# Kernel tuning notes

Measured on AMD Instinct MI355X. Metric: run time of the kernel, lower is better.

The kernel has to match this reference:

```python
import jax, jax.numpy as jnp
import numpy as np


def bilinear_resize(x, out_h, out_w):
    # x: [B, C, H, W]; matches torch F.interpolate(mode='bilinear', align_corners=False)
    B, C, H, W = x.shape
    ry = jnp.clip((jnp.arange(out_h, dtype=jnp.float32) + 0.5) * (H / out_h) - 0.5, 0.0, H - 1)
    rx = jnp.clip((jnp.arange(out_w, dtype=jnp.float32) + 0.5) * (W / out_w) - 0.5, 0.0, W - 1)
    y0 = jnp.floor(ry).astype(jnp.int32); y1 = jnp.minimum(y0 + 1, H - 1)
    x0 = jnp.floor(rx).astype(jnp.int32); x1 = jnp.minimum(x0 + 1, W - 1)
    wy = (ry - y0)[:, None]  # [out_h,1]
    wx = (rx - x0)[None, :]  # [1,out_w]
    r0 = x[:, :, y0, :]; r1 = x[:, :, y1, :]
    v00 = r0[:, :, :, x0]; v01 = r0[:, :, :, x1]
    v10 = r1[:, :, :, x0]; v11 = r1[:, :, :, x1]
    return (v00 * (1 - wx) + v01 * wx) * (1 - wy) + (v10 * (1 - wx) + v11 * wx) * wy


def setup_inputs() -> dict:
    key0 = jax.random.key(0)
    ks = jax.random.split(key0, 16)
    B, N, C, H = 2, 300, 256, 8
    hw_lvl = np.array([[64, 64], [32, 32], [16, 16]], dtype=np.int64)
    L = int((hw_lvl[:, 0] * hw_lvl[:, 1]).sum())  # 5376
    p = lambda k, sh: (0.02 * jax.random.normal(k, sh, dtype=jnp.float32))
    return {
        'query': jax.random.normal(ks[0], (B, N, C), dtype=jnp.float32),
        'key': jax.random.normal(ks[1], (B, L, C), dtype=jnp.float32),
        'value': jax.random.normal(ks[2], (B, L, C), dtype=jnp.float32),
        'key_padding_mask': jnp.zeros((B, L), dtype=bool),
        'hw_lvl': hw_lvl,
        'Wq': p(ks[3], (C, C)), 'Wk': p(ks[4], (C, C)), 'Wv': p(ks[5], (C, C)),
        'Wp': p(ks[6], (C, C)), 'bp': jnp.zeros((C,), jnp.float32),
        'W1': p(ks[7], (H, H)), 'b1': jnp.zeros((H,), jnp.float32),
        'W2': p(ks[8], (H, H)), 'b2': jnp.zeros((H,), jnp.float32),
        'W3': p(ks[9], (H, H)), 'b3': jnp.zeros((H,), jnp.float32),
        'Wm': p(ks[10], (3 * H, 1)), 'bm': jnp.zeros((1,), jnp.float32),
    }


def reference(query, key, value, key_padding_mask, hw_lvl,
              Wq, Wk, Wv, Wp, bp, W1, b1, W2, b2, W3, b3, Wm, bm):
    hw = np.asarray(hw_lvl)
    h1, wd1 = int(hw[0, 0]), int(hw[0, 1])
    h2, wd2 = int(hw[1, 0]), int(hw[1, 1])
    h3, wd3 = int(hw[2, 0]), int(hw[2, 1])
    w1 = h1 * wd1
    w2 = w1 + h2 * wd2
    B, N, C = query.shape
    L = key.shape[1]
    H = W1.shape[0]
    scale = (C // H) ** -0.5

    q = (query @ Wq).reshape(B, N, H, C // H)
    k = (key @ Wk).reshape(B, L, H, C // H)
    v = (value @ Wv).reshape(B, L, H, C // H)
    attn = jnp.einsum('bnhd,blhd->bhnl', q, k) * scale  # [B,H,N,L]

    ap = attn.transpose(0, 2, 3, 1)  # [B,N,L,H]
    f1 = jax.nn.relu(ap[:, :, :w1] @ W1 + b1)                      # [B,N,w1,H]
    f2 = jax.nn.relu(ap[:, :, w1:w2] @ W2 + b2)                    # [B,N,h2*wd2,H]
    f3 = jax.nn.relu(ap[:, :, w2:] @ W3 + b3)                      # [B,N,h3*wd3,H]
    f2 = f2.transpose(0, 1, 3, 2).reshape(B * N, H, h2, wd2)
    f3 = f3.transpose(0, 1, 3, 2).reshape(B * N, H, h3, wd3)
    f2 = bilinear_resize(f2, h1, wd1).transpose(0, 2, 3, 1).reshape(B, N, w1, H)
    f3 = bilinear_resize(f3, h1, wd1).transpose(0, 2, 3, 1).reshape(B, N, w1, H)
    new_feats = jnp.concatenate([f1, f2, f3], axis=-1)             # [B,N,w1,3H]
    mask = jax.nn.relu(new_feats @ Wm + bm)                        # [B,N,w1,1]

    aw = jax.nn.softmax(attn, axis=-1)                             # [B,H,N,L]
    x = jnp.einsum('bhnl,blhd->bnhd', aw, v).reshape(B, N, C)
    x = x @ Wp + bp
    return x, mask
```

## Files before the change

### kernel.cpp

```cpp
#include <hip/hip_runtime.h>
#include <hip/hip_bf16.h>

typedef __hip_bfloat16 bf16;
typedef __attribute__((ext_vector_type(8))) short short8v;
typedef __attribute__((ext_vector_type(8))) unsigned short ushort8v;
typedef __attribute__((ext_vector_type(4))) unsigned short ushort4v;
typedef __attribute__((ext_vector_type(4))) float float4v;

__device__ __forceinline__ float bfu2f(unsigned short u) {
    union { unsigned int i; float f; } v; v.i = ((unsigned int)u) << 16; return v.f;
}
__device__ __forceinline__ unsigned short f2bfu_rn(float x) {
    union { float f; unsigned int i; } u; u.f = x;
    unsigned int r = (u.i + 0x7FFFu + ((u.i >> 16) & 1u)) >> 16;
    return (unsigned short)r;
}

__global__ __launch_bounds__(256) void cast_wt(
    const float* __restrict__ Wq, const float* __restrict__ Wk,
    const float* __restrict__ Wv, const float* __restrict__ Wp,
    unsigned short* __restrict__ wt)
{
    __shared__ unsigned short tile[64][72];
    const float* W = (blockIdx.z == 0) ? Wq : (blockIdx.z == 1) ? Wk
                   : (blockIdx.z == 2) ? Wv : Wp;
    unsigned short* WT = wt + (size_t)blockIdx.z * 65536;
    const int t = threadIdx.x;
    const int k0 = blockIdx.x * 64, n0 = blockIdx.y * 64;
    {
        const int r = t >> 2, cseg = (t & 3) * 16;
        const float* src = W + (size_t)(k0 + r) * 256 + n0 + cseg;
        #pragma unroll
        for (int j = 0; j < 16; ++j) tile[r][cseg + j] = f2bfu_rn(src[j]);
    }
    __syncthreads();
    {
        const int ch = t & 63, lq = t >> 6;
        ushort8v o0, o1;
        #pragma unroll
        for (int i = 0; i < 8; ++i) o0[i] = tile[lq * 16 + i][ch];
        #pragma unroll
        for (int i = 0; i < 8; ++i) o1[i] = tile[lq * 16 + 8 + i][ch];
        unsigned short* dst = WT + (size_t)(n0 + ch) * 256 + k0 + lq * 16;
        *(ushort8v*)(dst)     = o0;
        *(ushort8v*)(dst + 8) = o1;
    }
}

__device__ __forceinline__ void proj_core(
    const float* __restrict__ aptr, const unsigned short* __restrict__ Wt,
    int nc0, int m16, int quad, float4v acc[8])
{
    #pragma unroll
    for (int i = 0; i < 8; ++i) acc[i] = (float4v){0.f, 0.f, 0.f, 0.f};
    #pragma unroll
    for (int ks = 0; ks < 8; ++ks) {
        float4 a0 = *(const float4*)(aptr + ks * 32);
        float4 a1 = *(const float4*)(aptr + ks * 32 + 4);
        short8v af;
        af[0] = (short)f2bfu_rn(a0.x); af[1] = (short)f2bfu_rn(a0.y);
        af[2] = (short)f2bfu_rn(a0.z); af[3] = (short)f2bfu_rn(a0.w);
        af[4] = (short)f2bfu_rn(a1.x); af[5] = (short)f2bfu_rn(a1.y);
        af[6] = (short)f2bfu_rn(a1.z); af[7] = (short)f2bfu_rn(a1.w);
        #pragma unroll
        for (int i = 0; i < 8; ++i) {
            short8v bfr = *(const short8v*)(Wt + (size_t)(nc0 + i * 16 + m16) * 256 + ks * 32 + quad * 8);
            acc[i] = __builtin_amdgcn_mfma_f32_16x16x32_bf16(af, bfr, acc[i], 0, 0, 0);
        }
    }
}

__global__ __launch_bounds__(256) void proj_all(
    const float* __restrict__ q, const float* __restrict__ k, const float* __restrict__ v,
    const unsigned short* __restrict__ wt,
    unsigned short* __restrict__ qb, unsigned short* __restrict__ kb,
    unsigned short* __restrict__ vt)
{
    const int t = threadIdx.x;
    const int wave = t >> 6, lane = t & 63;
    const int m16 = lane & 15, quad = lane >> 4;
    const int msub = (wave & 1) * 16;
    const int nc0 = (wave >> 1) * 128;
    const int bx = blockIdx.x;

    float4v acc[8];
    if (bx < 19) {
        const int m0 = bx * 32;
        const int arow = min(m0 + msub + m16, 599);
        proj_core(q + (size_t)arow * 256 + quad * 8, wt, nc0, m16, quad, acc);
        #pragma unroll
        for (int i = 0; i < 8; ++i)
            #pragma unroll
            for (int r = 0; r < 4; ++r) {
                int m = m0 + msub + quad * 4 + r;
                if (m < 600)
                    qb[(size_t)m * 256 + nc0 + i * 16 + m16] = f2bfu_rn(acc[i][r]);
            }
    } else if (bx < 355) {
        const int m0 = (bx - 19) * 32;
        proj_core(k + (size_t)(m0 + msub + m16) * 256 + quad * 8, wt + 65536, nc0, m16, quad, acc);
        #pragma unroll
        for (int i = 0; i < 8; ++i)
            #pragma unroll
            for (int r = 0; r < 4; ++r) {
                int m = m0 + msub + quad * 4 + r;
                kb[(size_t)m * 256 + nc0 + i * 16 + m16] = f2bfu_rn(acc[i][r]);
            }
    } else {
        const int m0 = (bx - 355) * 32;
        proj_core(v + (size_t)(m0 + msub + m16) * 256 + quad * 8, wt + 131072, nc0, m16, quad, acc);
        const int bb = (m0 >= 5376) ? 1 : 0;
        const int lcol = m0 - bb * 5376 + msub + quad * 4;
        #pragma unroll
        for (int i = 0; i < 8; ++i) {
            const int ch = nc0 + i * 16 + m16;
            ushort4v p;
            #pragma unroll
            for (int r = 0; r < 4; ++r) p[r] = f2bfu_rn(acc[i][r]);
            *(ushort4v*)(vt + (size_t)(bb * 256 + ch) * 5376 + lcol) = p;
        }
    }
}

__global__ __launch_bounds__(512) void attn_fused(
    const unsigned short* __restrict__ qb, const unsigned short* __restrict__ kb,
    const unsigned short* __restrict__ vt,
    unsigned short* __restrict__ attn, float* __restrict__ xbp, float* __restrict__ Sp)
{
    __shared__ unsigned short probs[8][16 * 104];
    __shared__ float partial[8][64][9];
    __shared__ float SrowP[8][16];

    const int t = threadIdx.x;
    const int wave = t >> 6, lane = t & 63;

    const int i0 = blockIdx.x;
    const int c = i0 & 7;
    int m = i0 >> 3;
    const int half = (m >= 133) ? 1 : 0;
    const int bh = c * 2 + half;
    m -= half * 133;
    const int n0 = (m % 19) * 16;
    const int zz = m / 19;

    const int b = bh >> 3, h = bh & 7;
    const int m16 = lane & 15, quad = lane >> 4;
    const float scale = 0.17677669529663687f;

    const unsigned short* qp = qb + (size_t)(b * 300 + min(n0 + m16, 299)) * 256 + h * 32 + quad * 8;
    const short8v qfrag = *(const short8v*)qp;

    const unsigned short* kbase = kb + (size_t)(b * 5376) * 256 + h * 32 + quad * 8;
    const unsigned short* vt0 = vt + (size_t)(b * 256 + h * 32 + m16) * 5376;
    const unsigned short* vt1 = vt0 + (size_t)16 * 5376;

    unsigned short* pw = &probs[wave][0];
    const int lc = zz * 768 + wave * 96;

    float4v c0 = {0.f, 0.f, 0.f, 0.f};
    float4v c1 = {0.f, 0.f, 0.f, 0.f};
    float sm = 0.f;

    #pragma unroll
    for (int i = 0; i < 6; ++i) {
        const int lcol = lc + i * 16 + m16;
        short8v kf = *(const short8v*)(kbase + (size_t)lcol * 256);
        float4v c = {0.f, 0.f, 0.f, 0.f};
        c = __builtin_amdgcn_mfma_f32_16x16x32_bf16(kf, qfrag, c, 0, 0, 0);
        ushort4v pk;
        #pragma unroll
        for (int r = 0; r < 4; ++r) pk[r] = f2bfu_rn(c[r] * scale);
        *(ushort4v*)(pw + m16 * 104 + i * 16 + quad * 4) = pk;
    }

    {
        const int row = lane >> 2;
        const int n = n0 + row;
        if (n < 300) {
            unsigned short* gdst = attn + ((size_t)(b * 300 + n) * 8 + h) * 5376 + lc;
            const unsigned short* lsrc = pw + row * 104;
            #pragma unroll
            for (int it = 0; it < 3; ++it) {
                const int colk = (lane & 3) * 8 + it * 32;
                *(ushort8v*)(gdst + colk) = *(const ushort8v*)(lsrc + colk);
            }
        }
    }

    #pragma unroll
    for (int step = 0; step < 3; ++step) {
        const int lloc = step * 32 + quad * 8;
        ushort8v ua = *(const ushort8v*)(pw + m16 * 104 + lloc);
        short8v af;
        #pragma unroll
        for (int j = 0; j < 8; ++j) {
            float e = __expf(bfu2f(ua[j]));
            sm += e;
            af[j] = (short)f2bfu_rn(e);
        }
        const int lg = lc + lloc;
        short8v b0 = *(const short8v*)(vt0 + lg);
        short8v b1 = *(const short8v*)(vt1 + lg);
        c0 = __builtin_amdgcn_mfma_f32_16x16x32_bf16(af, b0, c0, 0, 0, 0);
        c1 = __builtin_amdgcn_mfma_f32_16x16x32_bf16(af, b1, c1, 0, 0, 0);
    }

    sm += __shfl_xor(sm, 16);
    sm += __shfl_xor(sm, 32);
    if (lane < 16) SrowP[wave][lane] = sm;
    #pragma unroll
    for (int j = 0; j < 4; ++j) {
        partial[wave][lane][j]     = c0[j];
        partial[wave][lane][4 + j] = c1[j];
    }
    __syncthreads();

    if (t < 64) {
        float acc[8] = {0.f, 0.f, 0.f, 0.f, 0.f, 0.f, 0.f, 0.f};
        #pragma unroll
        for (int w = 0; w < 8; ++w)
            #pragma unroll
            for (int j = 0; j < 8; ++j) acc[j] += partial[w][t][j];

        const int d = t & 15, q = t >> 4;
        float* xplane = xbp + (size_t)zz * 153600;
        float* splane = Sp + (size_t)zz * 4800;
        #pragma unroll
        for (int r = 0; r < 4; ++r) {
            const int row = q * 4 + r;
            const int nn = n0 + row;
            if (nn < 300) {
                float S = 0.f;
                #pragma unroll
                for (int w = 0; w < 8; ++w) S += SrowP[w][row];
                if (d == 0) splane[(size_t)(b * 300 + nn) * 8 + h] = S;
                float* o = xplane + (size_t)(b * 300 + nn) * 256 + h * 32 + d;
                o[0]  = acc[r];
                o[16] = acc[4 + r];
            }
        }
    }
}

__global__ __launch_bounds__(256) void proj_out(
    const float* __restrict__ xbp, const float* __restrict__ Sp,
    const unsigned short* __restrict__ Wtp,
    const float* __restrict__ bp, float* __restrict__ out)
{
    const int t = threadIdx.x;
    const int wave = t >> 6, lane = t & 63;
    const int m16 = lane & 15, quad = lane >> 4;
    const int msub = (wave & 1) * 16;
    const int nc0 = (wave >> 1) * 128;
    const int m0 = blockIdx.x * 32;

    const int arow = min(m0 + msub + m16, 599);
    const float* a0p = xbp + (size_t)arow * 256 + quad * 8;

    float4v acc[8];
    #pragma unroll
    for (int i = 0; i < 8; ++i) acc[i] = (float4v){0.f, 0.f, 0.f, 0.f};

    #pragma unroll
    for (int ks = 0; ks < 8; ++ks) {
        float S = 0.f;
        #pragma unroll
        for (int z = 0; z < 7; ++z) S += Sp[(size_t)z * 4800 + (size_t)arow * 8 + ks];
        const float rS = 1.0f / S;
        float a[8];
        #pragma unroll
        for (int half = 0; half < 2; ++half) {
            const float* p = a0p + ks * 32 + half * 4;
            float sx = 0.f, sy = 0.f, sz = 0.f, sw = 0.f;
            #pragma unroll
            for (int z = 0; z < 7; ++z) {
                float4 x = *(const float4*)(p + (size_t)z * 153600);
                sx += x.x; sy += x.y; sz += x.z; sw += x.w;
            }
            a[half * 4 + 0] = sx * rS;
            a[half * 4 + 1] = sy * rS;
            a[half * 4 + 2] = sz * rS;
            a[half * 4 + 3] = sw * rS;
        }
        short8v af;
        #pragma unroll
        for (int j = 0; j < 8; ++j) af[j] = (short)f2bfu_rn(a[j]);
        #pragma unroll
        for (int i = 0; i < 8; ++i) {
            short8v bfr = *(const short8v*)(Wtp + (size_t)(nc0 + i * 16 + m16) * 256 + ks * 32 + quad * 8);
            acc[i] = __builtin_amdgcn_mfma_f32_16x16x32_bf16(af, bfr, acc[i], 0, 0, 0);
        }
    }

    #pragma unroll
    for (int i = 0; i < 8; ++i) {
        const float bv = bp[nc0 + i * 16 + m16];
        #pragma unroll
        for (int r = 0; r < 4; ++r) {
            int m = m0 + msub + quad * 4 + r;
            if (m < 600)
                out[(size_t)m * 256 + nc0 + i * 16 + m16] = acc[i][r] + bv;
        }
    }
}

__global__ __launch_bounds__(256) void mask_kernel(
    const bf16* __restrict__ attn,
    const float* __restrict__ W1, const float* __restrict__ b1,
    const float* __restrict__ W2, const float* __restrict__ b2,
    const float* __restrict__ W3, const float* __restrict__ b3,
    const float* __restrict__ Wm, const float* __restrict__ bmp,
    float* __restrict__ out)
{
    __shared__ float g2s[1024];
    __shared__ float g3s[256];
    __shared__ float w1s[64], w2s[64], w3s[64];
    __shared__ float b1s[8], b2s[8], b3s[8];
    __shared__ float wms[24];
    __shared__ float bms;

    const int t  = threadIdx.x;
    const int bn = blockIdx.x;
    const int ph = blockIdx.y;
    const unsigned short* ap = (const unsigned short*)attn + (size_t)bn * 8 * 5376;

    if (t < 64) { w1s[t] = W1[t]; w2s[t] = W2[t]; w3s[t] = W3[t]; }
    if (t < 8)  { b1s[t] = b1[t]; b2s[t] = b2[t]; b3s[t] = b3[t]; }
    if (t < 24) wms[t] = Wm[t];
    if (t == 0) bms = bmp[0];
    __syncthreads();

    {
        const int l2 = t * 4;
        ushort4v u[8];
        #pragma unroll
        for (int hh = 0; hh < 8; ++hh)
            u[hh] = *(const ushort4v*)(ap + hh * 5376 + 4096 + l2);
        #pragma unroll
        for (int pp = 0; pp < 4; ++pp) {
            float g = 0.f;
            #pragma unroll
            for (int hh = 0; hh < 8; ++hh) {
                float s = b2s[hh];
                #pragma unroll
                for (int hp = 0; hp < 8; ++hp) s += bfu2f(u[hp][pp]) * w2s[hp * 8 + hh];
                g += fmaxf(s, 0.f) * wms[8 + hh];
            }
            g2s[l2 + pp] = g;
        }
    }
    if (t < 64) {
        const int l3 = t * 4;
        ushort4v u[8];
        #pragma unroll
        for (int hh = 0; hh < 8; ++hh)
            u[hh] = *(const ushort4v*)(ap + hh * 5376 + 5120 + l3);
        #pragma unroll
        for (int pp = 0; pp < 4; ++pp) {
            float g = 0.f;
            #pragma unroll
            for (int hh = 0; hh < 8; ++hh) {
                float s = b3s[hh];
                #pragma unroll
                for (int hp = 0; hp < 8; ++hp) s += bfu2f(u[hp][pp]) * w3s[hp * 8 + hh];
                g += fmaxf(s, 0.f) * wms[16 + hh];
            }
            g3s[l3 + pp] = g;
        }
    }
    __syncthreads();

    {
        const int p0 = ph * 2048 + t * 8;
        ushort8v u[8];
        #pragma unroll
        for (int hh = 0; hh < 8; ++hh)
            u[hh] = *(const ushort8v*)(ap + hh * 5376 + p0);

        float res[8];
        #pragma unroll
        for (int pp = 0; pp < 8; ++pp) {
            const int p = p0 + pp;
            const int Y = p >> 6, X = p & 63;

            float acc = bms;
            #pragma unroll
            for (int hh = 0; hh < 8; ++hh) {
                float s = b1s[hh];
                #pragma unroll
                for (int hp = 0; hp < 8; ++hp) s += bfu2f(u[hp][pp]) * w1s[hp * 8 + hh];
                acc += fmaxf(s, 0.f) * wms[hh];
            }
            {
                float ry = fminf(fmaxf(0.5f * Y - 0.25f, 0.f), 31.f);
                float rx = fminf(fmaxf(0.5f * X - 0.25f, 0.f), 31.f);
                int y0 = (int)ry, x0 = (int)rx;
                int y1 = min(y0 + 1, 31), x1 = min(x0 + 1, 31);
                float wy = ry - (float)y0, wx = rx - (float)x0;
                acc += (g2s[y0 * 32 + x0] * (1.f - wx) + g2s[y0 * 32 + x1] * wx) * (1.f - wy)
                     + (g2s[y1 * 32 + x0] * (1.f - wx) + g2s[y1 * 32 + x1] * wx) * wy;
            }
            {
                float ry = fminf(fmaxf(0.25f * Y - 0.375f, 0.f), 15.f);
                float rx = fminf(fmaxf(0.25f * X - 0.375f, 0.f), 15.f);
                int y0 = (int)ry, x0 = (int)rx;
                int y1 = min(y0 + 1, 15), x1 = min(x0 + 1, 15);
                float wy = ry - (float)y0, wx = rx - (float)x0;
                acc += (g3s[y0 * 16 + x0] * (1.f - wx) + g3s[y0 * 16 + x1] * wx) * (1.f - wy)
                     + (g3s[y1 * 16 + x0] * (1.f - wx) + g3s[y1 * 16 + x1] * wx) * wy;
            }
            res[pp] = fmaxf(acc, 0.f);
        }
        float* o = out + 153600 + (size_t)bn * 4096 + p0;
        #pragma unroll
        for (int pp = 0; pp < 8; ++pp) o[pp] = res[pp];
    }
}

extern "C" void kernel_launch(void* const* d_in, const int* in_sizes, int n_in,
                              void* d_out, int out_size, void* d_ws, size_t ws_size,
                              hipStream_t stream) {
    const float* query = (const float*)d_in[0];
    const float* key   = (const float*)d_in[1];
    const float* value = (const float*)d_in[2];
    const float* Wq = (const float*)d_in[5];
    const float* Wk = (const float*)d_in[6];
    const float* Wv = (const float*)d_in[7];
    const float* Wp = (const float*)d_in[8];
    const float* bp = (const float*)d_in[9];
    const float* W1 = (const float*)d_in[10];
    const float* b1 = (const float*)d_in[11];
    const float* W2 = (const float*)d_in[12];
    const float* b2 = (const float*)d_in[13];
    const float* W3 = (const float*)d_in[14];
    const float* b3 = (const float*)d_in[15];
    const float* Wm = (const float*)d_in[16];
    const float* bm = (const float*)d_in[17];
    float* out = (float*)d_out;

    char* ws = (char*)d_ws;
    unsigned short* wt = (unsigned short*)(ws);
    bf16*  qb   = (bf16*) (ws + 524288);
    bf16*  kb   = (bf16*) (ws + 831488);
    bf16*  vt   = (bf16*) (ws + 6336512);
    bf16*  attn = (bf16*) (ws + 11841536);
    float* xbp  = (float*)(ws + 63451136);
    float* Sp   = (float*)(ws + 67751936);

    cast_wt<<<dim3(4, 4, 4), 256, 0, stream>>>(Wq, Wk, Wv, Wp, wt);

    proj_all<<<691, 256, 0, stream>>>(query, key, value, wt,
        (unsigned short*)qb, (unsigned short*)kb, (unsigned short*)vt);

    attn_fused<<<2128, 512, 0, stream>>>(
        (const unsigned short*)qb, (const unsigned short*)kb, (const unsigned short*)vt,
        (unsigned short*)attn, xbp, Sp);

    mask_kernel<<<dim3(600, 2), 256, 0, stream>>>(attn, W1, b1, W2, b2, W3, b3, Wm, bm, out);

    proj_out<<<19, 256, 0, stream>>>(xbp, Sp, (const unsigned short*)wt + 196608, bp, out);
}
```

Measured before the change: 216.3 us.

## Fuse per-position head-mixing MLP into attention kernel, drop bf16 attn tensor

The attention kernel now maps one head per wave, with 8 heads sharing a 16-query by 128-key tile. After the QK tile it does a cross-wave reduction over heads in shared memory and applies the 8x8 FC, ReLU and mask-weight dot in place. It writes compact fp32 per-position scalars (f1dot, gf) instead of the full bf16 attention matrix, which removes the large attn write and re-read by the mask kernel. The cost is 42 split-L partial planes instead of 7, so proj_out must reduce many more partial xbp and S planes, adding reads in its small 19-block launch.

```diff
diff --git a/kernel.cpp b/kernel.cpp
--- a/kernel.cpp
+++ b/kernel.cpp
@@ -125,27 +125,37 @@
 __global__ __launch_bounds__(512) void attn_fused(
     const unsigned short* __restrict__ qb, const unsigned short* __restrict__ kb,
     const unsigned short* __restrict__ vt,
-    unsigned short* __restrict__ attn, float* __restrict__ xbp, float* __restrict__ Sp)
-{
-    __shared__ unsigned short probs[8][16 * 104];
-    __shared__ float partial[8][64][9];
-    __shared__ float SrowP[8][16];
+    const float* __restrict__ W1, const float* __restrict__ b1,
+    const float* __restrict__ W2, const float* __restrict__ b2,
+    const float* __restrict__ W3, const float* __restrict__ b3,
+    const float* __restrict__ Wm, const float* __restrict__ bmp,
+    float* __restrict__ f1dot, float* __restrict__ gf,
+    float* __restrict__ xbp, float* __restrict__ Sp)
+{
+    const int STR = 134;
+    __shared__ unsigned short probs[8][16 * 134];
+    __shared__ float wfc[64], bfc[8], wmf[8];
+    __shared__ float bmsS;
 
     const int t = threadIdx.x;
     const int wave = t >> 6, lane = t & 63;
-
-    const int i0 = blockIdx.x;
-    const int c = i0 & 7;
-    int m = i0 >> 3;
-    const int half = (m >= 133) ? 1 : 0;
-    const int bh = c * 2 + half;
-    m -= half * 133;
-    const int n0 = (m % 19) * 16;
-    const int zz = m / 19;
-
-    const int b = bh >> 3, h = bh & 7;
+    const int n0 = blockIdx.x * 16;
+    const int b  = blockIdx.y;
+    const int zz = blockIdx.z;
+    const int h = wave;
     const int m16 = lane & 15, quad = lane >> 4;
+    const int lc = zz * 128;
     const float scale = 0.17677669529663687f;
+
+    {
+        const float* Wsel; const float* bsel; int wmoff;
+        if (zz < 32)      { Wsel = W1; bsel = b1; wmoff = 0; }
+        else if (zz < 40) { Wsel = W2; bsel = b2; wmoff = 8; }
+        else              { Wsel = W3; bsel = b3; wmoff = 16; }
+        if (t < 64) wfc[t] = Wsel[t];
+        if (t < 8)  { bfc[t] = bsel[t]; wmf[t] = Wm[wmoff + t]; }
+        if (t == 0) bmsS = bmp[0];
+    }
 
     const unsigned short* qp = qb + (size_t)(b * 300 + min(n0 + m16, 299)) * 256 + h * 32 + quad * 8;
     const short8v qfrag = *(const short8v*)qp;
@@ -153,16 +163,10 @@
     const unsigned short* kbase = kb + (size_t)(b * 5376) * 256 + h * 32 + quad * 8;
     const unsigned short* vt0 = vt + (size_t)(b * 256 + h * 32 + m16) * 5376;
     const unsigned short* vt1 = vt0 + (size_t)16 * 5376;
-
     unsigned short* pw = &probs[wave][0];
-    const int lc = zz * 768 + wave * 96;
-
-    float4v c0 = {0.f, 0.f, 0.f, 0.f};
-    float4v c1 = {0.f, 0.f, 0.f, 0.f};
-    float sm = 0.f;
-
-    #pragma unroll
-    for (int i = 0; i < 6; ++i) {
+
+    #pragma unroll
+    for (int i = 0; i < 8; ++i) {
         const int lcol = lc + i * 16 + m16;
         short8v kf = *(const short8v*)(kbase + (size_t)lcol * 256);
         float4v c = {0.f, 0.f, 0.f, 0.f};
@@ -170,27 +174,48 @@
         ushort4v pk;
         #pragma unroll
         for (int r = 0; r < 4; ++r) pk[r] = f2bfu_rn(c[r] * scale);
-        *(ushort4v*)(pw + m16 * 104 + i * 16 + quad * 4) = pk;
-    }
-
-    {
-        const int row = lane >> 2;
-        const int n = n0 + row;
-        if (n < 300) {
-            unsigned short* gdst = attn + ((size_t)(b * 300 + n) * 8 + h) * 5376 + lc;
-            const unsigned short* lsrc = pw + row * 104;
+        *(ushort4v*)(pw + m16 * STR + i * 16 + quad * 4) = pk;
+    }
+    __syncthreads();
+
+    {
+        const int n = t >> 5, lt = t & 31;
+        const int nn = n0 + n;
+        if (nn < 300) {
+            ushort4v u[8];
             #pragma unroll
-            for (int it = 0; it < 3; ++it) {
-                const int colk = (lane & 3) * 8 + it * 32;
-                *(ushort8v*)(gdst + colk) = *(const ushort8v*)(lsrc + colk);
-            }
-        }
-    }
-
-    #pragma unroll
-    for (int step = 0; step < 3; ++step) {
+            for (int hp = 0; hp < 8; ++hp)
+                u[hp] = *(const ushort4v*)(&probs[hp][0] + n * STR + lt * 4);
+            float4 o;
+            float* op = (float*)&o;
+            #pragma unroll
+            for (int j = 0; j < 4; ++j) {
+                float acc = (zz < 32) ? bmsS : 0.f;
+                #pragma unroll
+                for (int hh = 0; hh < 8; ++hh) {
+                    float s = bfc[hh];
+                    #pragma unroll
+                    for (int hp = 0; hp < 8; ++hp) s += bfu2f(u[hp][j]) * wfc[hp * 8 + hh];
+                    acc += fmaxf(s, 0.f) * wmf[hh];
+                }
+                op[j] = acc;
+            }
+            if (zz < 32) {
+                *(float4*)(f1dot + (size_t)(b * 300 + nn) * 4096 + lc + lt * 4) = o;
+            } else {
+                const int cell = lc - 4096 + lt * 4;
+                *(float4*)(gf + (size_t)(b * 300 + nn) * 1280 + cell) = o;
+            }
+        }
+    }
+
+    float4v c0 = {0.f, 0.f, 0.f, 0.f};
+    float4v c1 = {0.f, 0.f, 0.f, 0.f};
+    float sm = 0.f;
+    #pragma unroll
+    for (int step = 0; step < 4; ++step) {
         const int lloc = step * 32 + quad * 8;
-        ushort8v ua = *(const ushort8v*)(pw + m16 * 104 + lloc);
+        ushort8v ua = *(const ushort8v*)(pw + m16 * STR + lloc);
         short8v af;
         #pragma unroll
         for (int j = 0; j < 8; ++j) {
@@ -200,44 +225,28 @@
         }
         const int lg = lc + lloc;
         short8v b0 = *(const short8v*)(vt0 + lg);
-        short8v b1 = *(const short8v*)(vt1 + lg);
+        short8v b1v = *(const short8v*)(vt1 + lg);
         c0 = __builtin_amdgcn_mfma_f32_16x16x32_bf16(af, b0, c0, 0, 0, 0);
-        c1 = __builtin_amdgcn_mfma_f32_16x16x32_bf16(af, b1, c1, 0, 0, 0);
-    }
-
-    sm += __shfl_xor(sm, 16);
-    sm += __shfl_xor(sm, 32);
-    if (lane < 16) SrowP[wave][lane] = sm;
-    #pragma unroll
-    for (int j = 0; j < 4; ++j) {
-        partial[wave][lane][j]     = c0[j];
-        partial[wave][lane][4 + j] = c1[j];
-    }
-    __syncthreads();
-
-    if (t < 64) {
-        float acc[8] = {0.f, 0.f, 0.f, 0.f, 0.f, 0.f, 0.f, 0.f};
-        #pragma unroll
-        for (int w = 0; w < 8; ++w)
-            #pragma unroll
-            for (int j = 0; j < 8; ++j) acc[j] += partial[w][t][j];
-
-        const int d = t & 15, q = t >> 4;
+        c1 = __builtin_amdgcn_mfma_f32_16x16x32_bf16(af, b1v, c1, 0, 0, 0);
+    }
+
+    {
         float* xplane = xbp + (size_t)zz * 153600;
-        float* splane = Sp + (size_t)zz * 4800;
         #pragma unroll
         for (int r = 0; r < 4; ++r) {
-            const int row = q * 4 + r;
-            const int nn = n0 + row;
+            const int nn = n0 + quad * 4 + r;
             if (nn < 300) {
-                float S = 0.f;
-                #pragma unroll
-                for (int w = 0; w < 8; ++w) S += SrowP[w][row];
-                if (d == 0) splane[(size_t)(b * 300 + nn) * 8 + h] = S;
-                float* o = xplane + (size_t)(b * 300 + nn) * 256 + h * 32 + d;
-                o[0]  = acc[r];
-                o[16] = acc[4 + r];
-            }
+                float* o = xplane + (size_t)(b * 300 + nn) * 256 + h * 32 + m16;
+                o[0]  = c0[r];
+                o[16] = c1[r];
+            }
+        }
+        sm += __shfl_xor(sm, 16);
+        sm += __shfl_xor(sm, 32);
+        if (lane < 16) {
+            const int nn = n0 + lane;
+            if (nn < 300)
+                Sp[(size_t)zz * 4800 + (size_t)(b * 300 + nn) * 8 + h] = sm;
         }
     }
 }
@@ -247,6 +256,7 @@
     const unsigned short* __restrict__ Wtp,
     const float* __restrict__ bp, float* __restrict__ out)
 {
+    const int NZ = 42;
     const int t = threadIdx.x;
     const int wave = t >> 6, lane = t & 63;
     const int m16 = lane & 15, quad = lane >> 4;
@@ -264,16 +274,14 @@
     #pragma unroll
     for (int ks = 0; ks < 8; ++ks) {
         float S = 0.f;
-        #pragma unroll
-        for (int z = 0; z < 7; ++z) S += Sp[(size_t)z * 4800 + (size_t)arow * 8 + ks];
+        for (int z = 0; z < NZ; ++z) S += Sp[(size_t)z * 4800 + (size_t)arow * 8 + ks];
         const float rS = 1.0f / S;
         float a[8];
         #pragma unroll
         for (int half = 0; half < 2; ++half) {
             const float* p = a0p + ks * 32 + half * 4;
             float sx = 0.f, sy = 0.f, sz = 0.f, sw = 0.f;
-            #pragma unroll
-            for (int z = 0; z < 7; ++z) {
+            for (int z = 0; z < NZ; ++z) {
                 float4 x = *(const float4*)(p + (size_t)z * 153600);
                 sx += x.x; sy += x.y; sz += x.z; sw += x.w;
             }
@@ -304,117 +312,56 @@
     }
 }
 
-__global__ __launch_bounds__(256) void mask_kernel(
-    const bf16* __restrict__ attn,
-    const float* __restrict__ W1, const float* __restrict__ b1,
-    const float* __restrict__ W2, const float* __restrict__ b2,
-    const float* __restrict__ W3, const float* __restrict__ b3,
-    const float* __restrict__ Wm, const float* __restrict__ bmp,
+__global__ __launch_bounds__(256) void mask_lite(
+    const float* __restrict__ f1dot, const float* __restrict__ gf,
     float* __restrict__ out)
 {
-    __shared__ float g2s[1024];
-    __shared__ float g3s[256];
-    __shared__ float w1s[64], w2s[64], w3s[64];
-    __shared__ float b1s[8], b2s[8], b3s[8];
-    __shared__ float wms[24];
-    __shared__ float bms;
-
+    __shared__ float gs[1280];
     const int t  = threadIdx.x;
     const int bn = blockIdx.x;
     const int ph = blockIdx.y;
-    const unsigned short* ap = (const unsigned short*)attn + (size_t)bn * 8 * 5376;
-
-    if (t < 64) { w1s[t] = W1[t]; w2s[t] = W2[t]; w3s[t] = W3[t]; }
-    if (t < 8)  { b1s[t] = b1[t]; b2s[t] = b2[t]; b3s[t] = b3[t]; }
-    if (t < 24) wms[t] = Wm[t];
-    if (t == 0) bms = bmp[0];
+
+    {
+        const float4* src = (const float4*)(gf + (size_t)bn * 1280);
+        ((float4*)gs)[t] = src[t];
+        if (t < 64) ((float4*)gs)[256 + t] = src[256 + t];
+    }
     __syncthreads();
 
-    {
-        const int l2 = t * 4;
-        ushort4v u[8];
-        #pragma unroll
-        for (int hh = 0; hh < 8; ++hh)
-            u[hh] = *(const ushort4v*)(ap + hh * 5376 + 4096 + l2);
-        #pragma unroll
-        for (int pp = 0; pp < 4; ++pp) {
-            float g = 0.f;
-            #pragma unroll
-            for (int hh = 0; hh < 8; ++hh) {
-                float s = b2s[hh];
-                #pragma unroll
-                for (int hp = 0; hp < 8; ++hp) s += bfu2f(u[hp][pp]) * w2s[hp * 8 + hh];
-                g += fmaxf(s, 0.f) * wms[8 + hh];
-            }
-            g2s[l2 + pp] = g;
-        }
-    }
-    if (t < 64) {
-        const int l3 = t * 4;
-        ushort4v u[8];
-        #pragma unroll
-        for (int hh = 0; hh < 8; ++hh)
-            u[hh] = *(const ushort4v*)(ap + hh * 5376 + 5120 + l3);
-        #pragma unroll
-        for (int pp = 0; pp < 4; ++pp) {
-            float g = 0.f;
-            #pragma unroll
-            for (int hh = 0; hh < 8; ++hh) {
-                float s = b3s[hh];
-                #pragma unroll
-                for (int hp = 0; hp < 8; ++hp) s += bfu2f(u[hp][pp]) * w3s[hp * 8 + hh];
-                g += fmaxf(s, 0.f) * wms[16 + hh];
-            }
-            g3s[l3 + pp] = g;
-        }
-    }
-    __syncthreads();
-
-    {
-        const int p0 = ph * 2048 + t * 8;
-        ushort8v u[8];
-        #pragma unroll
-        for (int hh = 0; hh < 8; ++hh)
-            u[hh] = *(const ushort8v*)(ap + hh * 5376 + p0);
-
-        float res[8];
-        #pragma unroll
-        for (int pp = 0; pp < 8; ++pp) {
-            const int p = p0 + pp;
-            const int Y = p >> 6, X = p & 63;
-
-            float acc = bms;
-            #pragma unroll
-            for (int hh = 0; hh < 8; ++hh) {
-                float s = b1s[hh];
-                #pragma unroll
-                for (int hp = 0; hp < 8; ++hp) s += bfu2f(u[hp][pp]) * w1s[hp * 8 + hh];
-                acc += fmaxf(s, 0.f) * wms[hh];
-            }
-            {
-                float ry = fminf(fmaxf(0.5f * Y - 0.25f, 0.f), 31.f);
-                float rx = fminf(fmaxf(0.5f * X - 0.25f, 0.f), 31.f);
-                int y0 = (int)ry, x0 = (int)rx;
-                int y1 = min(y0 + 1, 31), x1 = min(x0 + 1, 31);
-                float wy = ry - (float)y0, wx = rx - (float)x0;
-                acc += (g2s[y0 * 32 + x0] * (1.f - wx) + g2s[y0 * 32 + x1] * wx) * (1.f - wy)
-                     + (g2s[y1 * 32 + x0] * (1.f - wx) + g2s[y1 * 32 + x1] * wx) * wy;
-            }
-            {
-                float ry = fminf(fmaxf(0.25f * Y - 0.375f, 0.f), 15.f);
-                float rx = fminf(fmaxf(0.25f * X - 0.375f, 0.f), 15.f);
-                int y0 = (int)ry, x0 = (int)rx;
-                int y1 = min(y0 + 1, 15), x1 = min(x0 + 1, 15);
-                float wy = ry - (float)y0, wx = rx - (float)x0;
-                acc += (g3s[y0 * 16 + x0] * (1.f - wx) + g3s[y0 * 16 + x1] * wx) * (1.f - wy)
-                     + (g3s[y1 * 16 + x0] * (1.f - wx) + g3s[y1 * 16 + x1] * wx) * wy;
-            }
-            res[pp] = fmaxf(acc, 0.f);
-        }
-        float* o = out + 153600 + (size_t)bn * 4096 + p0;
-        #pragma unroll
-        for (int pp = 0; pp < 8; ++pp) o[pp] = res[pp];
-    }
+    const int p0 = ph * 2048 + t * 8;
+    float f[8];
+    *(float4*)&f[0] = *(const float4*)(f1dot + (size_t)bn * 4096 + p0);
+    *(float4*)&f[4] = *(const float4*)(f1dot + (size_t)bn * 4096 + p0 + 4);
+
+    float res[8];
+    #pragma unroll
+    for (int pp = 0; pp < 8; ++pp) {
+        const int p = p0 + pp;
+        const int Y = p >> 6, X = p & 63;
+        float acc = f[pp];
+        {
+            float ry = fminf(fmaxf(0.5f * Y - 0.25f, 0.f), 31.f);
+            float rx = fminf(fmaxf(0.5f * X - 0.25f, 0.f), 31.f);
+            int y0 = (int)ry, x0 = (int)rx;
+            int y1 = min(y0 + 1, 31), x1 = min(x0 + 1, 31);
+            float wy = ry - (float)y0, wx = rx - (float)x0;
+            acc += (gs[y0 * 32 + x0] * (1.f - wx) + gs[y0 * 32 + x1] * wx) * (1.f - wy)
+                 + (gs[y1 * 32 + x0] * (1.f - wx) + gs[y1 * 32 + x1] * wx) * wy;
+        }
+        {
+            float ry = fminf(fmaxf(0.25f * Y - 0.375f, 0.f), 15.f);
+            float rx = fminf(fmaxf(0.25f * X - 0.375f, 0.f), 15.f);
+            int y0 = (int)ry, x0 = (int)rx;
+            int y1 = min(y0 + 1, 15), x1 = min(x0 + 1, 15);
+            float wy = ry - (float)y0, wx = rx - (float)x0;
+            acc += (gs[1024 + y0 * 16 + x0] * (1.f - wx) + gs[1024 + y0 * 16 + x1] * wx) * (1.f - wy)
+                 + (gs[1024 + y1 * 16 + x0] * (1.f - wx) + gs[1024 + y1 * 16 + x1] * wx) * wy;
+        }
+        res[pp] = fmaxf(acc, 0.f);
+    }
+    float* o = out + 153600 + (size_t)bn * 4096 + p0;
+    *(float4*)(o)     = *(float4*)&res[0];
+    *(float4*)(o + 4) = *(float4*)&res[4];
 }
 
 extern "C" void kernel_launch(void* const* d_in, const int* in_sizes, int n_in,
@@ -440,23 +387,25 @@
 
     char* ws = (char*)d_ws;
     unsigned short* wt = (unsigned short*)(ws);
-    bf16*  qb   = (bf16*) (ws + 524288);
-    bf16*  kb   = (bf16*) (ws + 831488);
-    bf16*  vt   = (bf16*) (ws + 6336512);
-    bf16*  attn = (bf16*) (ws + 11841536);
-    float* xbp  = (float*)(ws + 63451136);
-    float* Sp   = (float*)(ws + 67751936);
+    bf16*  qb    = (bf16*) (ws + 524288);
+    bf16*  kb    = (bf16*) (ws + 831488);
+    bf16*  vt    = (bf16*) (ws + 6336512);
+    float* f1dot = (float*)(ws + 11841536);
+    float* gf    = (float*)(ws + 21671936);
+    float* xbp   = (float*)(ws + 24743936);
+    float* Sp    = (float*)(ws + 50548736);
 
     cast_wt<<<dim3(4, 4, 4), 256, 0, stream>>>(Wq, Wk, Wv, Wp, wt);
 
     proj_all<<<691, 256, 0, stream>>>(query, key, value, wt,
         (unsigned short*)qb, (unsigned short*)kb, (unsigned short*)vt);
 
-    attn_fused<<<2128, 512, 0, stream>>>(
+    attn_fused<<<dim3(19, 2, 42), 512, 0, stream>>>(
         (const unsigned short*)qb, (const unsigned short*)kb, (const unsigned short*)vt,
-        (unsigned short*)attn, xbp, Sp);
-
-    mask_kernel<<<dim3(600, 2), 256, 0, stream>>>(attn, W1, b1, W2, b2, W3, b3, Wm, bm, out);
+        W1, b1, W2, b2, W3, b3, Wm, bm,
+        f1dot, gf, xbp, Sp);
+
+    mask_lite<<<dim3(600, 2), 256, 0, stream>>>(f1dot, gf, out);
 
     proj_out<<<19, 256, 0, stream>>>(xbp, Sp, (const unsigned short*)wt + 196608, bp, out);
 }
```

After: 375.1 us. +73.4%, slower.
